# Performance work log

Measured on AMD Instinct MI355X. Metric: run time of the kernel, lower is better.

The kernel has to match this reference:

```python
import jax, jax.numpy as jnp
import numpy as np

LN_EPS = 1e-5  # torch LayerNorm default

def _phi(x):
    # elu(x) + 1 feature map
    return jax.nn.elu(x) + 1.0

def setup_inputs() -> dict:
    key = jax.random.key(0)
    ks = jax.random.split(key, 5)
    B, N, D = 4, 8192, 1024
    s = 1.0 / np.sqrt(D)
    return {
        "H": jax.random.normal(ks[0], (B, N, D), dtype=jnp.float32),
        "W_qkv": jax.random.normal(ks[1], (3 * D, D), dtype=jnp.float32) * s,
        "b_qkv": jax.random.normal(ks[2], (3 * D,), dtype=jnp.float32) * 0.01,
        "W_proj": jax.random.normal(ks[3], (D, D), dtype=jnp.float32) * s,
        "b_proj": jax.random.normal(ks[4], (D,), dtype=jnp.float32) * 0.01,
        "gamma": jnp.ones((D,), dtype=jnp.float32),
        "beta": jnp.zeros((D,), dtype=jnp.float32),
    }

def reference(H, W_qkv, b_qkv, W_proj, b_proj, gamma, beta):
    B, N, D = H.shape
    num_heads = 16
    head_dim = D // num_heads
    residual = H
    # qkv projection: (B,N,3D)
    qkv = jnp.einsum('bnd,ed->bne', H, W_qkv) + b_qkv
    qkv = qkv.reshape(B, N, 3, num_heads, head_dim).transpose(2, 0, 3, 1, 4)
    q, k, v = qkv[0], qkv[1], qkv[2]  # each (B,h,N,d)
    q = _phi(q)
    k = _phi(k)
    # kv outer-product accumulated over nodes: (B,h,d,v)
    kv = jnp.einsum('bhnd,bhnv->bhdv', k, v)
    k1 = k.sum(axis=2)  # (B,h,d)
    qkv_out = jnp.einsum('bhnd,bhdv->bhnv', q, kv)
    qk1 = jnp.sum(q * k1[:, :, None, :], axis=-1, keepdims=True)
    out = qkv_out / jnp.clip(qk1, 1e-6, None)
    # NOTE: faithful to original -- reshape (B,h,N,d) -> (B,N,D) WITHOUT head transpose
    out = out.reshape(B, N, D)
    out = jnp.einsum('bnd,ed->bne', out, W_proj) + b_proj
    # LayerNorm over last dim
    mu = out.mean(axis=-1, keepdims=True)
    var = out.var(axis=-1, keepdims=True)
    out = (out - mu) * jax.lax.rsqrt(var + LN_EPS) * gamma + beta
    # dropout is identity at inference
    return out + residual
```

## Files before the change

### kernel.cpp

```cpp
#include <hip/hip_runtime.h>


typedef __attribute__((ext_vector_type(4))) float f32x4;
typedef __attribute__((ext_vector_type(8))) short bf16x8;

__device__ __forceinline__ unsigned short f2b(float f) {
    unsigned u = __float_as_uint(f);
    u = (u + 0x7FFFu + ((u >> 16) & 1u)) >> 16;
    return (unsigned short)u;
}
__device__ __forceinline__ float b2f(unsigned short h) {
    return __uint_as_float(((unsigned)h) << 16);
}

__device__ __forceinline__ void glds16(const void* gp, void* lp) {
    __builtin_amdgcn_global_load_lds(
        (__attribute__((address_space(1))) void*)(unsigned long long)gp,
        (__attribute__((address_space(3))) void*)(unsigned int)(unsigned long long)lp,
        16, 0, 0);
}

__global__ __launch_bounds__(256) void cvt_all(const float* __restrict__ H,
                                               const float* __restrict__ Wq,
                                               const float* __restrict__ Wp,
                                               unsigned short* __restrict__ hbf,
                                               unsigned short* __restrict__ wqb,
                                               unsigned short* __restrict__ wpb) {
    const int blk = blockIdx.x;
    const float* src; unsigned short* dst; long n4; int b0, nb;
    if (blk < 1792)      { src = H;  dst = hbf; n4 = 8388608; b0 = 0;    nb = 1792; }
    else if (blk < 1920) { src = Wq; dst = wqb; n4 = 786432;  b0 = 1792; nb = 128; }
    else                 { src = Wp; dst = wpb; n4 = 262144;  b0 = 1920; nb = 64; }
    long i = (long)(blk - b0) * 256 + threadIdx.x;
    const long stride = (long)nb * 256;
    for (; i < n4; i += stride) {
        float4 v = ((const float4*)src)[i];
        ushort4 o;
        o.x = f2b(v.x); o.y = f2b(v.y); o.z = f2b(v.z); o.w = f2b(v.w);
        ((ushort4*)dst)[i] = o;
    }
}

template<int MODE>
__global__ __launch_bounds__(512) void gemm256(const unsigned short* __restrict__ A,
                                               const unsigned short* __restrict__ B,
                                               const float* __restrict__ bias,
                                               void* __restrict__ Cout,
                                               int mb, int N, int K) {
    __shared__ unsigned short lds[2][2][256][64];
    const int tid = threadIdx.x;
    const int wid = tid >> 6, lane = tid & 63;
    const int wr = wid >> 2, wc = wid & 3;
    const int lr = lane & 15, lq = lane >> 4;
    const int cpx = (int)gridDim.x >> 3;
    const int L = ((int)blockIdx.x & 7) * cpx + ((int)blockIdx.x >> 3);
    const int nbv = N >> 8;
    const int gsz = 4 * nbv;
    const int g = L / gsz, r = L % gsz;
    const int bn = r >> 2;
    const int bm = g * 4 + (r & 3);
    const size_t aRow0 = (size_t)bm * 256, bRow0 = (size_t)bn * 256;

    const int sr8 = lane >> 3;
    const int ssw = ((lane & 7) ^ sr8) * 8;
    const unsigned short* aG = A + (aRow0 + (size_t)(wid * 8 + sr8)) * K + ssw;
    const unsigned short* bG = B + (bRow0 + (size_t)(wid * 8 + sr8)) * K + ssw;

    f32x4 acc[8][4] = {};
    const char* base = (const char*)&lds[0][0][0][0];

    auto stage = [&](int buf, int k0) {
#pragma unroll
        for (int j = 0; j < 8; ++j) {
            const unsigned short* g2 = (j < 4 ? aG : bG) + (size_t)(j & 3) * 64 * K + k0;
            glds16(g2, &lds[buf][j >> 2][(j & 3) * 64 + wid * 8][0]);
        }
    };
    auto ldA = [&](int cur, int mi, int ks) {
        int row = wr * 128 + mi * 16 + lr;
        int off = (cur * 2 + 0) * 32768 + row * 128 + ((((ks << 2) | lq) ^ (row & 7)) << 4);
        return *(const bf16x8*)(base + off);
    };
    auto ldB = [&](int cur, int ni, int ks) {
        int row = wc * 64 + ni * 16 + lr;
        int off = (cur * 2 + 1) * 32768 + row * 128 + ((((ks << 2) | lq) ^ (row & 7)) << 4);
        return *(const bf16x8*)(base + off);
    };

    const int nt = K >> 6;
    stage(0, 0);
    asm volatile("s_waitcnt vmcnt(0)" ::: "memory");
    __builtin_amdgcn_s_barrier();

    bf16x8 af[4][2], bfr[4][2];
    for (int t = 0; t < nt; ++t) {
        const int cur = t & 1;
#pragma unroll
        for (int mi = 0; mi < 4; ++mi) {
            af[mi][0] = ldA(cur, mi, 0); af[mi][1] = ldA(cur, mi, 1);
        }
#pragma unroll
        for (int ni = 0; ni < 2; ++ni) {
            bfr[ni][0] = ldB(cur, ni, 0); bfr[ni][1] = ldB(cur, ni, 1);
        }
        if (t + 1 < nt) stage(cur ^ 1, (t + 1) << 6);
        __builtin_amdgcn_s_barrier();
        __builtin_amdgcn_s_setprio(1);
#pragma unroll
        for (int mi = 0; mi < 4; ++mi)
#pragma unroll
            for (int ni = 0; ni < 2; ++ni)
#pragma unroll
                for (int ks = 0; ks < 2; ++ks)
                    acc[mi][ni] = __builtin_amdgcn_mfma_f32_16x16x32_bf16(
                        af[mi][ks], bfr[ni][ks], acc[mi][ni], 0, 0, 0);
        __builtin_amdgcn_s_setprio(0);
        __builtin_amdgcn_s_barrier();
#pragma unroll
        for (int ni = 2; ni < 4; ++ni) {
            bfr[ni][0] = ldB(cur, ni, 0); bfr[ni][1] = ldB(cur, ni, 1);
        }
        __builtin_amdgcn_s_barrier();
        __builtin_amdgcn_s_setprio(1);
#pragma unroll
        for (int mi = 0; mi < 4; ++mi)
#pragma unroll
            for (int ni = 2; ni < 4; ++ni)
#pragma unroll
                for (int ks = 0; ks < 2; ++ks)
                    acc[mi][ni] = __builtin_amdgcn_mfma_f32_16x16x32_bf16(
                        af[mi][ks], bfr[ni][ks], acc[mi][ni], 0, 0, 0);
        __builtin_amdgcn_s_setprio(0);
        __builtin_amdgcn_s_barrier();
#pragma unroll
        for (int mi = 0; mi < 4; ++mi) {
            af[mi][0] = ldA(cur, mi + 4, 0); af[mi][1] = ldA(cur, mi + 4, 1);
        }
        __builtin_amdgcn_s_barrier();
        __builtin_amdgcn_s_setprio(1);
#pragma unroll
        for (int mi = 0; mi < 4; ++mi)
#pragma unroll
            for (int ni = 2; ni < 4; ++ni)
#pragma unroll
                for (int ks = 0; ks < 2; ++ks)
                    acc[mi + 4][ni] = __builtin_amdgcn_mfma_f32_16x16x32_bf16(
                        af[mi][ks], bfr[ni][ks], acc[mi + 4][ni], 0, 0, 0);
        __builtin_amdgcn_s_setprio(0);
        __builtin_amdgcn_s_barrier();
        __builtin_amdgcn_s_setprio(1);
#pragma unroll
        for (int mi = 0; mi < 4; ++mi)
#pragma unroll
            for (int ni = 0; ni < 2; ++ni)
#pragma unroll
                for (int ks = 0; ks < 2; ++ks)
                    acc[mi + 4][ni] = __builtin_amdgcn_mfma_f32_16x16x32_bf16(
                        af[mi][ks], bfr[ni][ks], acc[mi + 4][ni], 0, 0, 0);
        __builtin_amdgcn_s_setprio(0);
        asm volatile("s_waitcnt vmcnt(0)" ::: "memory");
        __builtin_amdgcn_s_barrier();
        __builtin_amdgcn_sched_barrier(0);
    }
#pragma unroll
    for (int mi = 0; mi < 8; ++mi) {
#pragma unroll
        for (int ni = 0; ni < 4; ++ni) {
            int col = (int)bRow0 + wc * 64 + ni * 16 + lr;
            float bv = bias[col];
#pragma unroll
            for (int r2 = 0; r2 < 4; ++r2) {
                size_t row = aRow0 + wr * 128 + mi * 16 + lq * 4 + r2;
                float v = acc[mi][ni][r2] + bv;
                if (MODE == 0) {
                    if (col < 2048) v = (v > 0.f) ? (v + 1.f) : __expf(v);
                }
                ((unsigned short*)Cout)[row * (size_t)N + col] = f2b(v);
            }
        }
    }
}

__global__ __launch_bounds__(256) void kv_partial(const unsigned short* __restrict__ qkv,
                                                  float* __restrict__ part) {
    const int bh = blockIdx.x, chunk = blockIdx.y;
    const int b = bh >> 4, h = bh & 15;
    __shared__ float kbf[16][68];
    __shared__ float vbf[16][68];
    const int tid = threadIdx.x;
    const int d0 = (tid >> 4) * 4, v0 = (tid & 15) * 4;
    float acc[4][4] = {};
    float k1a[4] = {0.f, 0.f, 0.f, 0.f};
    const size_t base = ((size_t)b * 8192 + (size_t)chunk * 1024) * 3072;
    const int nn = tid >> 4;
    const int which = (tid >> 3) & 1;
    const int cg = tid & 7;
    const size_t loff = base + (size_t)nn * 3072 + (which ? 2048 : 1024) + h * 64 + cg * 8;

    for (int n0 = 0; n0 < 1024; n0 += 16) {
        uint4 val = *(const uint4*)(qkv + loff + (size_t)n0 * 3072);
        float* dst = (which ? &vbf[nn][0] : &kbf[nn][0]) + cg * 8;
        const unsigned short* us = (const unsigned short*)&val;
        float4 f0 = {b2f(us[0]), b2f(us[1]), b2f(us[2]), b2f(us[3])};
        float4 f1 = {b2f(us[4]), b2f(us[5]), b2f(us[6]), b2f(us[7])};
        *(float4*)(dst) = f0;
        *(float4*)(dst + 4) = f1;
        __syncthreads();
#pragma unroll 4
        for (int j = 0; j < 16; ++j) {
            float4 kd = *(const float4*)(&kbf[j][d0]);
            float4 vd = *(const float4*)(&vbf[j][v0]);
            acc[0][0] += kd.x * vd.x; acc[0][1] += kd.x * vd.y; acc[0][2] += kd.x * vd.z; acc[0][3] += kd.x * vd.w;
            acc[1][0] += kd.y * vd.x; acc[1][1] += kd.y * vd.y; acc[1][2] += kd.y * vd.z; acc[1][3] += kd.y * vd.w;
            acc[2][0] += kd.z * vd.x; acc[2][1] += kd.z * vd.y; acc[2][2] += kd.z * vd.z; acc[2][3] += kd.z * vd.w;
            acc[3][0] += kd.w * vd.x; acc[3][1] += kd.w * vd.y; acc[3][2] += kd.w * vd.z; acc[3][3] += kd.w * vd.w;
            if ((tid & 15) == 0) {
                k1a[0] += kd.x; k1a[1] += kd.y; k1a[2] += kd.z; k1a[3] += kd.w;
            }
        }
        __syncthreads();
    }
    float* dst = part + ((size_t)bh * 8 + chunk) * 4160;
#pragma unroll
    for (int i = 0; i < 4; ++i)
#pragma unroll
        for (int jj = 0; jj < 4; ++jj)
            dst[(v0 + jj) * 64 + d0 + i] = acc[i][jj];
    if ((tid & 15) == 0)
#pragma unroll
        for (int i = 0; i < 4; ++i) dst[4096 + d0 + i] = k1a[i];
}

__global__ __launch_bounds__(256) void kv_finish(const float* __restrict__ part,
                                                 unsigned short* __restrict__ kvbf,
                                                 float* __restrict__ k1f) {
    const int bh = blockIdx.x;
    const float* src = part + (size_t)bh * 8 * 4160;
    for (int i = threadIdx.x; i < 4096; i += 256) {
        float s = 0.f;
#pragma unroll
        for (int c = 0; c < 8; ++c) s += src[c * 4160 + i];
        kvbf[(size_t)bh * 4096 + i] = f2b(s);
    }
    if (threadIdx.x < 64) {
        float s = 0.f;
#pragma unroll
        for (int c = 0; c < 8; ++c) s += src[c * 4160 + 4096 + threadIdx.x];
        k1f[bh * 64 + threadIdx.x] = s;
    }
}

__global__ __launch_bounds__(256) void apply_attn(const unsigned short* __restrict__ qkv,
                                                  const unsigned short* __restrict__ kvbf,
                                                  const float* __restrict__ k1f,
                                                  unsigned short* __restrict__ att) {
    const int nblk = blockIdx.x;
    const int bh = blockIdx.y;
    const int b = bh >> 4, h = bh & 15;
    __shared__ unsigned short kvs[64][64];
    __shared__ float k1s[64];
    __shared__ float qk1s[64];
    const int tid = threadIdx.x;
    {
        const int v = tid >> 3, s = tid & 7;
        const uint4* srcv = (const uint4*)(kvbf + (size_t)bh * 4096);
#pragma unroll
        for (int half = 0; half < 2; ++half) {
            int vv = v + half * 32;
            uint4 val = srcv[vv * 8 + s];
            *(uint4*)(&kvs[vv][(s ^ (vv & 7)) * 8]) = val;
        }
        if (tid < 64) k1s[tid] = k1f[bh * 64 + tid];
    }
    __syncthreads();
    const int n0 = nblk * 64;
    const size_t qbase = ((size_t)b * 8192 + n0) * 3072 + h * 64;
    {
        const int row = tid >> 2, dq = (tid & 3) * 16;
        const unsigned short* qp = qkv + qbase + (size_t)row * 3072 + dq;
        float s = 0.f;
#pragma unroll
        for (int g2 = 0; g2 < 2; ++g2) {
            ushort4 u0 = *(const ushort4*)(qp + g2 * 8);
            ushort4 u1 = *(const ushort4*)(qp + g2 * 8 + 4);
            const float* kp = &k1s[dq + g2 * 8];
            s += b2f(u0.x) * kp[0] + b2f(u0.y) * kp[1] + b2f(u0.z) * kp[2] + b2f(u0.w) * kp[3]
               + b2f(u1.x) * kp[4] + b2f(u1.y) * kp[5] + b2f(u1.z) * kp[6] + b2f(u1.w) * kp[7];
        }
        s += __shfl_xor(s, 1, 64);
        s += __shfl_xor(s, 2, 64);
        if ((tid & 3) == 0) qk1s[row] = s;
    }
    __syncthreads();
    const int w = tid >> 6, lane = tid & 63;
    const int lr = lane & 15, lq = lane >> 4;
    bf16x8 af[2];
#pragma unroll
    for (int ks = 0; ks < 2; ++ks)
        af[ks] = *(const bf16x8*)(qkv + qbase + (size_t)(w * 16 + lr) * 3072 + ks * 32 + lq * 8);
    f32x4 acc[4] = {};
#pragma unroll
    for (int ni = 0; ni < 4; ++ni)
#pragma unroll
        for (int ks = 0; ks < 2; ++ks) {
            int v = ni * 16 + lr;
            bf16x8 bf = *(const bf16x8*)(&kvs[v][(((ks << 2) | lq) ^ (v & 7)) * 8]);
            acc[ni] = __builtin_amdgcn_mfma_f32_16x16x32_bf16(af[ks], bf, acc[ni], 0, 0, 0);
        }
    unsigned short* dstrow = att + (((size_t)b * 8192) + h * 512 + nblk * 4 + w) * 1024;
#pragma unroll
    for (int r = 0; r < 4; ++r) {
        float rinv = 1.f / fmaxf(qk1s[w * 16 + lq * 4 + r], 1e-6f);
#pragma unroll
        for (int ni = 0; ni < 4; ++ni)
            dstrow[(lq * 4 + r) * 64 + ni * 16 + lr] = f2b(acc[ni][r] * rinv);
    }
}

__global__ __launch_bounds__(256) void ln_residual(const unsigned short* __restrict__ X,
                                                   const float* __restrict__ H,
                                                   const float* __restrict__ gamma,
                                                   const float* __restrict__ beta,
                                                   float* __restrict__ out,
                                                   int nrows) {
    const int lane = threadIdx.x & 63;
    int row = blockIdx.x * 4 + (threadIdx.x >> 6);
    const int rstride = gridDim.x * 4;
    for (; row < nrows; row += rstride) {
        const unsigned short* x = X + (size_t)row * 1024;
        float v[16];
        float s = 0.f, s2 = 0.f;
#pragma unroll
        for (int j = 0; j < 4; ++j) {
            ushort4 u = *(const ushort4*)(x + j * 256 + lane * 4);
            float a = b2f(u.x), b = b2f(u.y), c = b2f(u.z), d = b2f(u.w);
            v[j * 4 + 0] = a; v[j * 4 + 1] = b; v[j * 4 + 2] = c; v[j * 4 + 3] = d;
            s += a + b + c + d;
            s2 += a * a + b * b + c * c + d * d;
        }
#pragma unroll
        for (int o = 32; o > 0; o >>= 1) {
            s  += __shfl_xor(s, o, 64);
            s2 += __shfl_xor(s2, o, 64);
        }
        const float mu = s * (1.f / 1024.f);
        const float var = s2 * (1.f / 1024.f) - mu * mu;
        const float inv = rsqrtf(var + 1e-5f);
        const float* hrow = H + (size_t)row * 1024;
        float* orow = out + (size_t)row * 1024;
#pragma unroll
        for (int j = 0; j < 4; ++j) {
            const int c = j * 256 + lane * 4;
            float4 g = *(const float4*)(gamma + c);
            float4 bt = *(const float4*)(beta + c);
            float4 hr = *(const float4*)(hrow + c);
            float4 o;
            o.x = (v[j * 4 + 0] - mu) * inv * g.x + bt.x + hr.x;
            o.y = (v[j * 4 + 1] - mu) * inv * g.y + bt.y + hr.y;
            o.z = (v[j * 4 + 2] - mu) * inv * g.z + bt.z + hr.z;
            o.w = (v[j * 4 + 3] - mu) * inv * g.w + bt.w + hr.w;
            *(float4*)(orow + c) = o;
        }
    }
}

extern "C" void kernel_launch(void* const* d_in, const int* in_sizes, int n_in,
                              void* d_out, int out_size, void* d_ws, size_t ws_size,
                              hipStream_t stream) {
    const float* H     = (const float*)d_in[0];
    const float* Wqkv  = (const float*)d_in[1];
    const float* bqkv  = (const float*)d_in[2];
    const float* Wproj = (const float*)d_in[3];
    const float* bproj = (const float*)d_in[4];
    const float* gamma = (const float*)d_in[5];
    const float* beta  = (const float*)d_in[6];
    float* out = (float*)d_out;
    char* ws = (char*)d_ws;

    unsigned short* wq_bf = (unsigned short*)(ws);
    unsigned short* wp_bf = (unsigned short*)(ws + 6291456);
    unsigned short* hbf   = (unsigned short*)(ws + 8388608);
    unsigned short* att   = hbf;
    unsigned short* qkvbf = (unsigned short*)(ws + 75497472);
    unsigned short* out2  = (unsigned short*)(ws + 75497472);
    unsigned short* kvbf  = (unsigned short*)(ws + 276824064);
    float*          k1f   = (float*)(ws + 277348352);
    float*          part  = (float*)(ws + 277889024);

    cvt_all<<<1984, 256, 0, stream>>>(H, Wqkv, Wproj, hbf, wq_bf, wp_bf);

    gemm256<0><<<1536, 512, 0, stream>>>(hbf, wq_bf, bqkv, (void*)qkvbf,
                                         128, 3072, 1024);

    kv_partial<<<dim3(64, 8), 256, 0, stream>>>(qkvbf, part);
    kv_finish<<<64, 256, 0, stream>>>(part, kvbf, k1f);

    apply_attn<<<dim3(128, 64), 256, 0, stream>>>(qkvbf, kvbf, k1f, att);

    gemm256<1><<<512, 512, 0, stream>>>(att, wp_bf, bproj, (void*)out2,
                                        128, 1024, 1024);

    ln_residual<<<2048, 256, 0, stream>>>(out2, H, gamma, beta, out, 32768);
}
```

Baseline: 536.3 us.

## Split QKV output into separate Q/K/V planes and read bf16 residual

The QKV GEMM epilogue now writes Q, K and V into three separate contiguous [B*N,1024] buffers instead of one interleaved 3072-wide buffer. kv_partial and apply_attn read these dense planes with stride 1024, which improves locality of their row accesses. The LayerNorm residual add now reads the bf16 copy of H instead of the fp32 original, halving that read traffic. The cost is that the residual loses precision, since bf16 H is added to the fp32 output.

```diff
diff --git a/kernel.cpp b/kernel.cpp
--- a/kernel.cpp
+++ b/kernel.cpp
@@ -174,14 +174,19 @@
                 float v = acc[mi][ni][r2] + bv;
                 if (MODE == 0) {
                     if (col < 2048) v = (v > 0.f) ? (v + 1.f) : __expf(v);
+                    size_t idx = ((size_t)(col >> 10)) * 33554432
+                                 + row * 1024 + (col & 1023);
+                    ((unsigned short*)Cout)[idx] = f2b(v);
+                } else {
+                    ((unsigned short*)Cout)[row * (size_t)N + col] = f2b(v);
                 }
-                ((unsigned short*)Cout)[row * (size_t)N + col] = f2b(v);
             }
         }
     }
 }
 
-__global__ __launch_bounds__(256) void kv_partial(const unsigned short* __restrict__ qkv,
+__global__ __launch_bounds__(256) void kv_partial(const unsigned short* __restrict__ kbuf,
+                                                  const unsigned short* __restrict__ vbuf,
                                                   float* __restrict__ part) {
     const int bh = blockIdx.x, chunk = blockIdx.y;
     const int b = bh >> 4, h = bh & 15;
@@ -191,14 +196,15 @@
     const int d0 = (tid >> 4) * 4, v0 = (tid & 15) * 4;
     float acc[4][4] = {};
     float k1a[4] = {0.f, 0.f, 0.f, 0.f};
-    const size_t base = ((size_t)b * 8192 + (size_t)chunk * 1024) * 3072;
     const int nn = tid >> 4;
     const int which = (tid >> 3) & 1;
     const int cg = tid & 7;
-    const size_t loff = base + (size_t)nn * 3072 + (which ? 2048 : 1024) + h * 64 + cg * 8;
+    const size_t loff = ((size_t)b * 8192 + (size_t)chunk * 1024 + nn) * 1024
+                        + h * 64 + cg * 8;
+    const unsigned short* src0 = which ? vbuf : kbuf;
 
     for (int n0 = 0; n0 < 1024; n0 += 16) {
-        uint4 val = *(const uint4*)(qkv + loff + (size_t)n0 * 3072);
+        uint4 val = *(const uint4*)(src0 + loff + (size_t)n0 * 1024);
         float* dst = (which ? &vbf[nn][0] : &kbf[nn][0]) + cg * 8;
         const unsigned short* us = (const unsigned short*)&val;
         float4 f0 = {b2f(us[0]), b2f(us[1]), b2f(us[2]), b2f(us[3])};
@@ -250,7 +256,7 @@
     }
 }
 
-__global__ __launch_bounds__(256) void apply_attn(const unsigned short* __restrict__ qkv,
+__global__ __launch_bounds__(256) void apply_attn(const unsigned short* __restrict__ qbuf,
                                                   const unsigned short* __restrict__ kvbf,
                                                   const float* __restrict__ k1f,
                                                   unsigned short* __restrict__ att) {
@@ -274,10 +280,10 @@
     }
     __syncthreads();
     const int n0 = nblk * 64;
-    const size_t qbase = ((size_t)b * 8192 + n0) * 3072 + h * 64;
+    const size_t qbase = ((size_t)b * 8192 + n0) * 1024 + h * 64;
     {
         const int row = tid >> 2, dq = (tid & 3) * 16;
-        const unsigned short* qp = qkv + qbase + (size_t)row * 3072 + dq;
+        const unsigned short* qp = qbuf + qbase + (size_t)row * 1024 + dq;
         float s = 0.f;
 #pragma unroll
         for (int g2 = 0; g2 < 2; ++g2) {
@@ -297,7 +303,7 @@
     bf16x8 af[2];
 #pragma unroll
     for (int ks = 0; ks < 2; ++ks)
-        af[ks] = *(const bf16x8*)(qkv + qbase + (size_t)(w * 16 + lr) * 3072 + ks * 32 + lq * 8);
+        af[ks] = *(const bf16x8*)(qbuf + qbase + (size_t)(w * 16 + lr) * 1024 + ks * 32 + lq * 8);
     f32x4 acc[4] = {};
 #pragma unroll
     for (int ni = 0; ni < 4; ++ni)
@@ -318,7 +324,7 @@
 }
 
 __global__ __launch_bounds__(256) void ln_residual(const unsigned short* __restrict__ X,
-                                                   const float* __restrict__ H,
+                                                   const unsigned short* __restrict__ Hb,
                                                    const float* __restrict__ gamma,
                                                    const float* __restrict__ beta,
                                                    float* __restrict__ out,
@@ -346,19 +352,19 @@
         const float mu = s * (1.f / 1024.f);
         const float var = s2 * (1.f / 1024.f) - mu * mu;
         const float inv = rsqrtf(var + 1e-5f);
-        const float* hrow = H + (size_t)row * 1024;
+        const unsigned short* hrow = Hb + (size_t)row * 1024;
         float* orow = out + (size_t)row * 1024;
 #pragma unroll
         for (int j = 0; j < 4; ++j) {
             const int c = j * 256 + lane * 4;
             float4 g = *(const float4*)(gamma + c);
             float4 bt = *(const float4*)(beta + c);
-            float4 hr = *(const float4*)(hrow + c);
+            ushort4 hu = *(const ushort4*)(hrow + c);
             float4 o;
-            o.x = (v[j * 4 + 0] - mu) * inv * g.x + bt.x + hr.x;
-            o.y = (v[j * 4 + 1] - mu) * inv * g.y + bt.y + hr.y;
-            o.z = (v[j * 4 + 2] - mu) * inv * g.z + bt.z + hr.z;
-            o.w = (v[j * 4 + 3] - mu) * inv * g.w + bt.w + hr.w;
+            o.x = (v[j * 4 + 0] - mu) * inv * g.x + bt.x + b2f(hu.x);
+            o.y = (v[j * 4 + 1] - mu) * inv * g.y + bt.y + b2f(hu.y);
+            o.z = (v[j * 4 + 2] - mu) * inv * g.z + bt.z + b2f(hu.z);
+            o.w = (v[j * 4 + 3] - mu) * inv * g.w + bt.w + b2f(hu.w);
             *(float4*)(orow + c) = o;
         }
     }
@@ -380,25 +386,27 @@
     unsigned short* wq_bf = (unsigned short*)(ws);
     unsigned short* wp_bf = (unsigned short*)(ws + 6291456);
     unsigned short* hbf   = (unsigned short*)(ws + 8388608);
-    unsigned short* att   = hbf;
-    unsigned short* qkvbf = (unsigned short*)(ws + 75497472);
-    unsigned short* out2  = (unsigned short*)(ws + 75497472);
+    unsigned short* qbuf  = (unsigned short*)(ws + 75497472);
+    unsigned short* kbuf  = (unsigned short*)(ws + 142606336);
+    unsigned short* vbuf  = (unsigned short*)(ws + 209715200);
+    unsigned short* att   = kbuf;
+    unsigned short* out2  = vbuf;
     unsigned short* kvbf  = (unsigned short*)(ws + 276824064);
     float*          k1f   = (float*)(ws + 277348352);
     float*          part  = (float*)(ws + 277889024);
 
     cvt_all<<<1984, 256, 0, stream>>>(H, Wqkv, Wproj, hbf, wq_bf, wp_bf);
 
-    gemm256<0><<<1536, 512, 0, stream>>>(hbf, wq_bf, bqkv, (void*)qkvbf,
+    gemm256<0><<<1536, 512, 0, stream>>>(hbf, wq_bf, bqkv, (void*)qbuf,
                                          128, 3072, 1024);
 
-    kv_partial<<<dim3(64, 8), 256, 0, stream>>>(qkvbf, part);
+    kv_partial<<<dim3(64, 8), 256, 0, stream>>>(kbuf, vbuf, part);
     kv_finish<<<64, 256, 0, stream>>>(part, kvbf, k1f);
 
-    apply_attn<<<dim3(128, 64), 256, 0, stream>>>(qkvbf, kvbf, k1f, att);
+    apply_attn<<<dim3(128, 64), 256, 0, stream>>>(qbuf, kvbf, k1f, att);
 
     gemm256<1><<<512, 512, 0, stream>>>(att, wp_bf, bproj, (void*)out2,
                                         128, 1024, 1024);
 
-    ln_residual<<<2048, 256, 0, stream>>>(out2, H, gamma, beta, out, 32768);
-}
+    ln_residual<<<2048, 256, 0, stream>>>(out2, hbf, gamma, beta, out, 32768);
+}
```

Measured after the change: 522.9 us. -2.5%, faster.
